# Kernel optimization log

Hardware: AMD Instinct MI355X
Metric: run time of the kernel (lower is better)

The kernel has to match this reference:

```python
import jax, jax.numpy as jnp
import numpy as np

N_NODES = 50000
N_EDGES = 1_600_000
F_IN = 32
HIDDEN = 32
HORIZON = 12
K = 2


def setup_inputs() -> dict:
    key = jax.random.key(0)
    ks = jax.random.split(key, 12)
    s = 0.1  # keep gates away from saturation
    x = jax.random.normal(ks[0], (N_NODES, 1, F_IN), dtype=jnp.float32)
    edge_index = jax.random.randint(ks[1], (2, N_EDGES), 0, N_NODES, dtype=jnp.int64)
    edge_weight = jax.random.uniform(ks[2], (N_EDGES,), dtype=jnp.float32)
    Wx = jax.random.normal(ks[3], (4, K, F_IN, HIDDEN), dtype=jnp.float32) * s
    bx = jax.random.normal(ks[4], (4, HIDDEN), dtype=jnp.float32) * s
    Wh = jax.random.normal(ks[5], (4, K, HIDDEN, HIDDEN), dtype=jnp.float32) * s
    bh = jax.random.normal(ks[6], (4, HIDDEN), dtype=jnp.float32) * s
    wc = jax.random.normal(ks[7], (3, HIDDEN), dtype=jnp.float32) * s
    b = jax.random.normal(ks[8], (4, HIDDEN), dtype=jnp.float32) * s
    W_lin = jax.random.normal(ks[9], (HIDDEN, HORIZON), dtype=jnp.float32) * s
    b_lin = jax.random.normal(ks[10], (HORIZON,), dtype=jnp.float32) * s
    h0 = jnp.zeros((N_NODES, HIDDEN), dtype=jnp.float32)
    c0 = jnp.zeros((N_NODES, HIDDEN), dtype=jnp.float32)
    return dict(x=x, edge_index=edge_index, edge_weight=edge_weight, Wx=Wx, bx=bx,
                Wh=Wh, bh=bh, wc=wc, b=b, W_lin=W_lin, b_lin=b_lin, h0=h0, c0=c0)


def reference(x, edge_index, edge_weight, Wx, bx, Wh, bh, wc, b, W_lin, b_lin, h0, c0):
    N = x.shape[0]
    src, dst = edge_index[0], edge_index[1]
    # ChebConv sym normalization with lambda_max=2: L_hat = L - I = -D^{-1/2} A D^{-1/2}
    deg = jax.ops.segment_sum(edge_weight, src, num_segments=N)
    dinv = jnp.where(deg > 0, jax.lax.rsqrt(deg), 0.0)
    nw = -dinv[src] * edge_weight * dinv[dst]  # [E]

    X = x[:, 0, :]  # squeeze(1) -> [N, F]

    def cheb(Z, W, bb):
        # K=2 Chebyshev: T0(Z)=Z, T1(Z)=L_hat Z (sparse gather-scatter)
        LZ = jax.ops.segment_sum(nw[:, None] * Z[src], dst, num_segments=N)
        return Z @ W[0] + LZ @ W[1] + bb

    # gate order: i, f, c, o
    I = jax.nn.sigmoid(cheb(X, Wx[0], bx[0]) + cheb(h0, Wh[0], bh[0]) + wc[0] * c0 + b[0])
    Fg = jax.nn.sigmoid(cheb(X, Wx[1], bx[1]) + cheb(h0, Wh[1], bh[1]) + wc[1] * c0 + b[1])
    T = jnp.tanh(cheb(X, Wx[2], bx[2]) + cheb(h0, Wh[2], bh[2]) + b[2])
    C = Fg * c0 + I * T
    O = jax.nn.sigmoid(cheb(X, Wx[3], bx[3]) + cheb(h0, Wh[3], bh[3]) + wc[2] * C + b[3])
    H = O * jnp.tanh(C)

    h = jax.nn.relu(H) @ W_lin + b_lin  # Linear(32, horizon)
    return (h, H, C)
```

## Files before the change

### kernel.cpp

```cpp
#include <hip/hip_runtime.h>
#include <math.h>

#define HID 32
#define HOR 12
#define NB  256
#define GSH 6
#define GW  64
#define NPT 4

__device__ __forceinline__ float sigmoidf_(float x) { return 1.0f / (1.0f + expf(-x)); }


__global__ __launch_bounds__(1024) void k_hist(const int* __restrict__ src,
                                               const int* __restrict__ dst,
                                               int* __restrict__ hist,
                                               int E, int chunk, int ng) {
    __shared__ int hS[1024], hD[1024];
    int t = threadIdx.x, b = blockIdx.x;
    for (int i = t; i < ng; i += 1024) { hS[i] = 0; hD[i] = 0; }
    __syncthreads();
    int beg = b * chunk, end = min(E, beg + chunk);
    for (int e = beg + t; e < end; e += 1024) {
        atomicAdd(&hS[src[e] >> GSH], 1);
        atomicAdd(&hD[dst[e] >> GSH], 1);
    }
    __syncthreads();
    for (int i = t; i < ng; i += 1024) {
        hist[(size_t)i * NB + b] = hS[i];
        hist[((size_t)ng + i) * NB + b] = hD[i];
    }
}

__global__ __launch_bounds__(256) void k_binscan(const int* __restrict__ hist,
                                                 int* __restrict__ off,
                                                 int* __restrict__ binTot, int ng2) {
    __shared__ int s[256];
    int b2 = blockIdx.x, t = threadIdx.x;
    int v = hist[(size_t)b2 * NB + t];
    s[t] = v;
    __syncthreads();
    for (int o = 1; o < 256; o <<= 1) {
        int x = (t >= o) ? s[t - o] : 0;
        __syncthreads();
        s[t] += x;
        __syncthreads();
    }
    off[(size_t)t * ng2 + b2] = s[t] - v;
    if (t == 255) binTot[b2] = s[255];
}

__global__ __launch_bounds__(1024) void k_binbase(const int* __restrict__ binTot,
                                                  int* __restrict__ baseS, int* __restrict__ baseD,
                                                  int* __restrict__ rowptr,
                                                  int E, int ng, int N) {
    __shared__ int buf[1024];
    int t = threadIdx.x;
    int isD = blockIdx.x;
    int sum = (t < ng) ? binTot[isD * ng + t] : 0;
    buf[t] = sum;
    __syncthreads();
    for (int o = 1; o < 1024; o <<= 1) {
        int v = (t >= o) ? buf[t - o] : 0;
        __syncthreads();
        buf[t] += v;
        __syncthreads();
    }
    int base = buf[t] - sum;
    int* B = isD ? baseD : baseS;
    if (t < ng) B[t] = base;
    if (t == 0) { B[ng] = E; if (!isD) rowptr[N] = E; }
}

__global__ __launch_bounds__(1024) void k_scatter(const int* __restrict__ src,
                                                  const int* __restrict__ dst,
                                                  const float* __restrict__ w,
                                                  const int* __restrict__ off,
                                                  const int* __restrict__ baseS,
                                                  const int* __restrict__ baseD,
                                                  int2* __restrict__ tmpS, int2* __restrict__ tmpD,
                                                  int E, int chunk, int ng) {
    __shared__ int cS[1024], cD[1024];
    int t = threadIdx.x, b = blockIdx.x;
    int ng2 = 2 * ng;
    for (int i = t; i < ng; i += 1024) {
        cS[i] = off[(size_t)b * ng2 + i] + baseS[i];
        cD[i] = off[(size_t)b * ng2 + ng + i] + baseD[i];
    }
    __syncthreads();
    int beg = b * chunk, end = min(E, beg + chunk);
    for (int e = beg + t; e < end; e += 1024) {
        int s = src[e], d = dst[e];
        int wb = __float_as_int(w[e]);
        int pS = atomicAdd(&cS[s >> GSH], 1);
        tmpS[pS] = make_int2(s, wb);
        int pD = atomicAdd(&cD[d >> GSH], 1);
        tmpD[pD] = make_int2(s | ((d & (GW - 1)) << 16), wb);
    }
}

__global__ __launch_bounds__(256) void k_degsum(const int2* __restrict__ tmpS,
                                                const int* __restrict__ baseS,
                                                float* __restrict__ dinv, int N) {
    __shared__ float h[GW];
    int g = blockIdx.x, t = threadIdx.x;
    if (t < GW) h[t] = 0.0f;
    __syncthreads();
    int beg = baseS[g], end = baseS[g + 1];
    for (int i = beg + t; i < end; i += 256) {
        int2 p = tmpS[i];
        atomicAdd(&h[p.x & (GW - 1)], __int_as_float(p.y));
    }
    __syncthreads();
    int n = (g << GSH) + t;
    if (t < GW && n < N) { float s = h[t]; dinv[n] = (s > 0.0f) ? rsqrtf(s) : 0.0f; }
}

__global__ __launch_bounds__(256) void k_scatter2(const int2* __restrict__ tmpD,
                                                  const int* __restrict__ baseD,
                                                  const float* __restrict__ dinv,
                                                  int* __restrict__ rowptr,
                                                  int2* __restrict__ epair, int N) {
    __shared__ int h[GW], cur[GW];
    int g = blockIdx.x, t = threadIdx.x;
    if (t < GW) h[t] = 0;
    __syncthreads();
    int beg = baseD[g], end = baseD[g + 1];
    for (int i = beg + t; i < end; i += 256) atomicAdd(&h[(tmpD[i].x >> 16) & (GW - 1)], 1);
    __syncthreads();
    int v = (t < GW) ? h[t] : 0;
    for (int o = 1; o < GW; o <<= 1) {
        int x = (t < GW && t >= o) ? h[t - o] : 0;
        __syncthreads();
        if (t < GW && t >= o) h[t] += x;
        __syncthreads();
    }
    if (t < GW) {
        int excl = h[t] - v;
        int n = (g << GSH) + t;
        if (n < N) rowptr[n] = beg + excl;
        cur[t] = beg + excl;
    }
    __syncthreads();
    for (int i = beg + t; i < end; i += 256) {
        int2 p = tmpD[i];
        int low = (p.x >> 16) & (GW - 1);
        int s = p.x & 0xFFFF;
        int pos = atomicAdd(&cur[low], 1);
        float nw = -dinv[s] * __int_as_float(p.y) * dinv[(g << GSH) + low];
        epair[pos] = make_int2(s, __float_as_int(nw));
    }
}

__global__ void k_flags(const float* __restrict__ h0, const float* __restrict__ c0,
                        int* __restrict__ flag, int total) {
    int i = blockIdx.x * 256 + threadIdx.x;
    float a = (i < total) ? h0[i] : 0.0f;
    float c = (i < total) ? c0[i] : 0.0f;
    unsigned long long ba = __ballot(a != 0.0f);
    unsigned long long bc = __ballot(c != 0.0f);
    if ((threadIdx.x & 63) == 0) {
        int m = (ba ? 1 : 0) | (bc ? 2 : 0);
        if (m) atomicOr(flag, m);
    }
}

__global__ __launch_bounds__(256) void k_gather(const int* __restrict__ rowptr,
                                                const int2* __restrict__ epair,
                                                const float* __restrict__ X,
                                                const float* __restrict__ H0,
                                                const int* __restrict__ hflag,
                                                float* __restrict__ LX, float* __restrict__ LH,
                                                int N) {
    int tid = blockIdx.x * 256 + threadIdx.x;
    int n = tid >> 5;
    int f = tid & 31;
    if (n >= N) return;
    int beg = rowptr[n], end = rowptr[n + 1];
    float acc = 0.0f, accH = 0.0f;
    int fl = *hflag;
    if (fl & 1) {
        #pragma unroll 4
        for (int i = beg; i < end; ++i) {
            int2 p = epair[i];
            float w = __int_as_float(p.y);
            acc  += w * X[(p.x << 5) + f];
            accH += w * H0[(p.x << 5) + f];
        }
    } else {
        #pragma unroll 4
        for (int i = beg; i < end; ++i) {
            int2 p = epair[i];
            acc += __int_as_float(p.y) * X[(p.x << 5) + f];
        }
    }
    LX[(n << 5) + f] = acc;
    if (fl & 1) LH[(n << 5) + f] = accH;
}

__global__ __launch_bounds__(256) void k_gates(
    const float* __restrict__ X, const float* __restrict__ LX,
    const float* __restrict__ H0, const float* __restrict__ LH,
    const float* __restrict__ C0,
    const float* __restrict__ Wx, const float* __restrict__ bx,
    const float* __restrict__ Wh, const float* __restrict__ bh,
    const float* __restrict__ wc, const float* __restrict__ b,
    const int* __restrict__ flag,
    float* __restrict__ outH, float* __restrict__ outC, int N) {
    int tid = blockIdx.x * 256 + threadIdx.x;
    int g = tid >> 5;
    int j = tid & 31;
    int n0 = g * NPT;
    if (n0 >= N) return;
    int cnt = min(NPT, N - n0);
    int f2 = *flag;

    if (f2 == 0) {
        float xk[NPT], lxk[NPT];
        #pragma unroll
        for (int i = 0; i < NPT; ++i) { xk[i] = 0.0f; lxk[i] = 0.0f; }
        for (int i = 0; i < cnt; ++i) {
            int base = (n0 + i) << 5;
            xk[i]  = X[base + j];
            lxk[i] = LX[base + j];
        }
        float p0[NPT], p2[NPT], p3[NPT];
        float b0 = bx[0 * HID + j] + bh[0 * HID + j] + b[0 * HID + j];
        float b2 = bx[2 * HID + j] + bh[2 * HID + j] + b[2 * HID + j];
        float b3 = bx[3 * HID + j] + bh[3 * HID + j] + b[3 * HID + j];
        #pragma unroll
        for (int i = 0; i < NPT; ++i) { p0[i] = b0; p2[i] = b2; p3[i] = b3; }

        #pragma unroll 4
        for (int k = 0; k < HID; ++k) {
            int row = k * HID + j;
            float w00 = Wx[0 * 2048 + row], w01 = Wx[0 * 2048 + 1024 + row];
            float w20 = Wx[2 * 2048 + row], w21 = Wx[2 * 2048 + 1024 + row];
            float w30 = Wx[3 * 2048 + row], w31 = Wx[3 * 2048 + 1024 + row];
            #pragma unroll
            for (int i = 0; i < NPT; ++i) {
                float xv  = __shfl(xk[i],  k, 32);
                float lxv = __shfl(lxk[i], k, 32);
                p0[i] += xv * w00 + lxv * w01;
                p2[i] += xv * w20 + lxv * w21;
                p3[i] += xv * w30 + lxv * w31;
            }
        }

        float wc2 = wc[2 * HID + j];
        for (int i = 0; i < cnt; ++i) {
            int base = (n0 + i) << 5;
            float I = sigmoidf_(p0[i]);
            float T = tanhf(p2[i]);
            float C = I * T;
            float O = sigmoidf_(p3[i] + wc2 * C);
            outH[base + j] = O * tanhf(C);
            outC[base + j] = C;
        }
        return;
    }

    float xk[NPT], lxk[NPT], hk[NPT], lhk[NPT];
    #pragma unroll
    for (int i = 0; i < NPT; ++i) { xk[i] = 0.0f; lxk[i] = 0.0f; hk[i] = 0.0f; lhk[i] = 0.0f; }
    for (int i = 0; i < cnt; ++i) {
        int base = (n0 + i) << 5;
        xk[i]  = X[base + j];
        lxk[i] = LX[base + j];
        hk[i]  = H0[base + j];
        lhk[i] = (f2 & 1) ? LH[base + j] : 0.0f;
    }

    float pre[4][NPT];
    #pragma unroll
    for (int gt = 0; gt < 4; ++gt) {
        float bb = bx[gt * HID + j] + bh[gt * HID + j] + b[gt * HID + j];
        #pragma unroll
        for (int i = 0; i < NPT; ++i) pre[gt][i] = bb;
    }

    #pragma unroll 2
    for (int k = 0; k < HID; ++k) {
        float w0[4], w1[4], w2[4], w3[4];
        int row = k * HID + j;
        #pragma unroll
        for (int gt = 0; gt < 4; ++gt) {
            w0[gt] = Wx[gt * 2048 + row];
            w1[gt] = Wx[gt * 2048 + 1024 + row];
            w2[gt] = Wh[gt * 2048 + row];
            w3[gt] = Wh[gt * 2048 + 1024 + row];
        }
        #pragma unroll
        for (int i = 0; i < NPT; ++i) {
            float xv  = __shfl(xk[i],  k, 32);
            float lxv = __shfl(lxk[i], k, 32);
            float hv  = __shfl(hk[i],  k, 32);
            float lhv = __shfl(lhk[i], k, 32);
            #pragma unroll
            for (int gt = 0; gt < 4; ++gt)
                pre[gt][i] += xv * w0[gt] + lxv * w1[gt] + hv * w2[gt] + lhv * w3[gt];
        }
    }

    float wc0 = wc[0 * HID + j], wc1 = wc[1 * HID + j], wc2 = wc[2 * HID + j];
    for (int i = 0; i < cnt; ++i) {
        int base = (n0 + i) << 5;
        float c0v = C0[base + j];
        float I  = sigmoidf_(pre[0][i] + wc0 * c0v);
        float Fg = sigmoidf_(pre[1][i] + wc1 * c0v);
        float T  = tanhf(pre[2][i]);
        float C  = Fg * c0v + I * T;
        float O  = sigmoidf_(pre[3][i] + wc2 * C);
        float H  = O * tanhf(C);
        outH[base + j] = H;
        outC[base + j] = C;
    }
}

__global__ void k_head(const float* __restrict__ H, const float* __restrict__ Wl,
                       const float* __restrict__ bl, float* __restrict__ hout, int N) {
    int tid = blockIdx.x * 256 + threadIdx.x;
    int n = tid / HOR;
    int t = tid - n * HOR;
    if (n >= N) return;
    float acc = bl[t];
    #pragma unroll
    for (int k = 0; k < HID; ++k) {
        float v = H[(n << 5) + k];
        acc += fmaxf(v, 0.0f) * Wl[k * HOR + t];
    }
    hout[n * HOR + t] = acc;
}

extern "C" void kernel_launch(void* const* d_in, const int* in_sizes, int n_in,
                              void* d_out, int out_size, void* d_ws, size_t ws_size,
                              hipStream_t stream) {
    const float* x  = (const float*)d_in[0];
    const int*   ei = (const int*)d_in[1];
    const float* ew = (const float*)d_in[2];
    const float* Wx = (const float*)d_in[3];
    const float* bx = (const float*)d_in[4];
    const float* Wh = (const float*)d_in[5];
    const float* bh = (const float*)d_in[6];
    const float* wc = (const float*)d_in[7];
    const float* b  = (const float*)d_in[8];
    const float* Wl = (const float*)d_in[9];
    const float* bl = (const float*)d_in[10];
    const float* h0 = (const float*)d_in[11];
    const float* c0 = (const float*)d_in[12];

    int N = in_sizes[0] / HID;
    int E = in_sizes[2];
    const int* src = ei;
    const int* dst = ei + E;

    int ng = (N + GW - 1) >> GSH;
    int ng2 = 2 * ng;
    int chunk = (E + NB - 1) / NB;

    int* wsi = (int*)d_ws;
    int2*  tmpD   = (int2*)wsi;
    int2*  tmpS   = (int2*)(wsi + 2 * (size_t)E);
    int2*  epair  = tmpS;
    float* LX     = (float*)(wsi + 4 * (size_t)E);
    float* LH     = LX + (size_t)N * HID;
    int*   rowptr = (int*)(LH + (size_t)N * HID);
    int*   hist   = rowptr + (N + 1);
    int*   off    = hist + (size_t)ng2 * NB;
    int*   binTot = off + (size_t)ng2 * NB;
    int*   baseS  = binTot + 2048;
    int*   baseD  = baseS + (ng + 1);
    float* dinv   = (float*)(baseD + (ng + 1));
    int*   flag   = (int*)(dinv + N);

    float* hOut = (float*)d_out;
    float* HOut = hOut + (size_t)N * HOR;
    float* COut = HOut + (size_t)N * HID;

    hipMemsetAsync(flag, 0, sizeof(int), stream);

    k_hist<<<NB, 1024, 0, stream>>>(src, dst, hist, E, chunk, ng);
    k_binscan<<<ng2, 256, 0, stream>>>(hist, off, binTot, ng2);
    k_binbase<<<2, 1024, 0, stream>>>(binTot, baseS, baseD, rowptr, E, ng, N);
    k_scatter<<<NB, 1024, 0, stream>>>(src, dst, ew, off, baseS, baseD, tmpS, tmpD, E, chunk, ng);
    k_degsum<<<ng, 256, 0, stream>>>(tmpS, baseS, dinv, N);
    k_flags<<<(N * HID + 255) / 256, 256, 0, stream>>>(h0, c0, flag, N * HID);
    k_scatter2<<<ng, 256, 0, stream>>>(tmpD, baseD, dinv, rowptr, epair, N);

    k_gather<<<(N * HID + 255) / 256, 256, 0, stream>>>(rowptr, epair, x, h0, flag, LX, LH, N);

    int gThreads = ((N + NPT - 1) / NPT) * 32;
    k_gates<<<(gThreads + 255) / 256, 256, 0, stream>>>(x, LX, h0, LH, c0,
                                                        Wx, bx, Wh, bh, wc, b, flag,
                                                        HOut, COut, N);

    k_head<<<(N * HOR + 255) / 256, 256, 0, stream>>>(HOut, Wl, bl, hOut, N);
}
```

Baseline: 275.5 us.

## Stage edge scatter in LDS tiles and gather per node-group with shared atomics

The edge bucketing kernel now sorts each 4096-edge tile in shared memory by group before writing it out, so global writes to each bin are contiguous rather than scattered one at a time. The second-level per-node scatter kernel is removed. The gather now runs one block per 64-node group, computing normalized weights on the fly and accumulating into shared-memory tiles with LDS float atomics. This drops a full pass over the edge list and the rowptr construction, at the cost of shared atomic contention and lower parallelism in the gather (one block per group, 8 edges in flight per block).

```diff
diff --git a/kernel.cpp b/kernel.cpp
--- a/kernel.cpp
+++ b/kernel.cpp
@@ -7,6 +7,10 @@
 #define GSH 6
 #define GW  64
 #define NPT 4
+#define TILE 4096
+#define TPB  256
+#define U    16
+#define BINS 1024
 
 __device__ __forceinline__ float sigmoidf_(float x) { return 1.0f / (1.0f + expf(-x)); }
 
@@ -15,7 +19,7 @@
                                                const int* __restrict__ dst,
                                                int* __restrict__ hist,
                                                int E, int chunk, int ng) {
-    __shared__ int hS[1024], hD[1024];
+    __shared__ int hS[BINS], hD[BINS];
     int t = threadIdx.x, b = blockIdx.x;
     for (int i = t; i < ng; i += 1024) { hS[i] = 0; hD[i] = 0; }
     __syncthreads();
@@ -51,8 +55,7 @@
 
 __global__ __launch_bounds__(1024) void k_binbase(const int* __restrict__ binTot,
                                                   int* __restrict__ baseS, int* __restrict__ baseD,
-                                                  int* __restrict__ rowptr,
-                                                  int E, int ng, int N) {
+                                                  int E, int ng) {
     __shared__ int buf[1024];
     int t = threadIdx.x;
     int isD = blockIdx.x;
@@ -68,33 +71,93 @@
     int base = buf[t] - sum;
     int* B = isD ? baseD : baseS;
     if (t < ng) B[t] = base;
-    if (t == 0) { B[ng] = E; if (!isD) rowptr[N] = E; }
-}
-
-__global__ __launch_bounds__(1024) void k_scatter(const int* __restrict__ src,
-                                                  const int* __restrict__ dst,
-                                                  const float* __restrict__ w,
-                                                  const int* __restrict__ off,
-                                                  const int* __restrict__ baseS,
-                                                  const int* __restrict__ baseD,
-                                                  int2* __restrict__ tmpS, int2* __restrict__ tmpD,
-                                                  int E, int chunk, int ng) {
-    __shared__ int cS[1024], cD[1024];
+    if (t == 0) B[ng] = E;
+}
+
+__global__ __launch_bounds__(256) void k_scatter(const int* __restrict__ src,
+                                                 const int* __restrict__ dst,
+                                                 const float* __restrict__ w,
+                                                 const int* __restrict__ off,
+                                                 const int* __restrict__ baseS,
+                                                 const int* __restrict__ baseD,
+                                                 int2* __restrict__ tmpS, int2* __restrict__ tmpD,
+                                                 int E, int chunk, int ng) {
+    __shared__ int2 stage[TILE];
+    __shared__ unsigned short stageG[TILE];
+    __shared__ int cnt[BINS];
+    __shared__ int gcur[BINS];
+    __shared__ int aux[TPB];
     int t = threadIdx.x, b = blockIdx.x;
+    int beg = b * chunk, end = min(E, beg + chunk);
     int ng2 = 2 * ng;
-    for (int i = t; i < ng; i += 1024) {
-        cS[i] = off[(size_t)b * ng2 + i] + baseS[i];
-        cD[i] = off[(size_t)b * ng2 + ng + i] + baseD[i];
-    }
-    __syncthreads();
-    int beg = b * chunk, end = min(E, beg + chunk);
-    for (int e = beg + t; e < end; e += 1024) {
-        int s = src[e], d = dst[e];
-        int wb = __float_as_int(w[e]);
-        int pS = atomicAdd(&cS[s >> GSH], 1);
-        tmpS[pS] = make_int2(s, wb);
-        int pD = atomicAdd(&cD[d >> GSH], 1);
-        tmpD[pD] = make_int2(s | ((d & (GW - 1)) << 16), wb);
+
+    for (int pass = 0; pass < 2; ++pass) {
+        for (int i = t; i < ng; i += TPB)
+            gcur[i] = (pass == 0) ? off[(size_t)b * ng2 + i] + baseS[i]
+                                  : off[(size_t)b * ng2 + ng + i] + baseD[i];
+        __syncthreads();
+
+        for (int tb = beg; tb < end; tb += TILE) {
+            int tcount = min(TILE, end - tb);
+            for (int i = t; i < BINS; i += TPB) cnt[i] = 0;
+            __syncthreads();
+
+            int g_[U], r_[U];
+            int2 p_[U];
+            #pragma unroll
+            for (int u = 0; u < U; ++u) {
+                int li = u * TPB + t;
+                g_[u] = -1;
+                if (li < tcount) {
+                    int e = tb + li;
+                    int s = src[e];
+                    int wb = __float_as_int(w[e]);
+                    int g; int2 p;
+                    if (pass == 0) { g = s >> GSH; p = make_int2(s, wb); }
+                    else { int d = dst[e]; g = d >> GSH; p = make_int2(s | ((d & (GW - 1)) << 16), wb); }
+                    g_[u] = g; p_[u] = p;
+                    r_[u] = atomicAdd(&cnt[g], 1);
+                }
+            }
+            __syncthreads();
+
+            int c0 = cnt[4 * t], c1 = cnt[4 * t + 1], c2 = cnt[4 * t + 2], c3 = cnt[4 * t + 3];
+            int q1 = c0, q2 = c0 + c1, q3 = c0 + c1 + c2, tsum = q3 + c3;
+            aux[t] = tsum;
+            __syncthreads();
+            for (int o = 1; o < TPB; o <<= 1) {
+                int v = (t >= o) ? aux[t - o] : 0;
+                __syncthreads();
+                aux[t] += v;
+                __syncthreads();
+            }
+            int excl = aux[t] - tsum;
+            cnt[4 * t] = excl; cnt[4 * t + 1] = excl + q1;
+            cnt[4 * t + 2] = excl + q2; cnt[4 * t + 3] = excl + q3;
+            __syncthreads();
+
+            #pragma unroll
+            for (int u = 0; u < U; ++u) {
+                if (g_[u] >= 0) {
+                    int pos = cnt[g_[u]] + r_[u];
+                    stage[pos] = p_[u];
+                    stageG[pos] = (unsigned short)g_[u];
+                }
+            }
+            __syncthreads();
+
+            int2* out = (pass == 0) ? tmpS : tmpD;
+            for (int i = t; i < tcount; i += TPB) {
+                int g = stageG[i];
+                out[gcur[g] + (i - cnt[g])] = stage[i];
+            }
+            __syncthreads();
+
+            gcur[4 * t] += c0; gcur[4 * t + 1] += c1;
+            gcur[4 * t + 2] += c2; gcur[4 * t + 3] += c3;
+            __syncthreads();
+        }
+        __syncthreads();
     }
 }
 
@@ -113,42 +176,6 @@
     __syncthreads();
     int n = (g << GSH) + t;
     if (t < GW && n < N) { float s = h[t]; dinv[n] = (s > 0.0f) ? rsqrtf(s) : 0.0f; }
-}
-
-__global__ __launch_bounds__(256) void k_scatter2(const int2* __restrict__ tmpD,
-                                                  const int* __restrict__ baseD,
-                                                  const float* __restrict__ dinv,
-                                                  int* __restrict__ rowptr,
-                                                  int2* __restrict__ epair, int N) {
-    __shared__ int h[GW], cur[GW];
-    int g = blockIdx.x, t = threadIdx.x;
-    if (t < GW) h[t] = 0;
-    __syncthreads();
-    int beg = baseD[g], end = baseD[g + 1];
-    for (int i = beg + t; i < end; i += 256) atomicAdd(&h[(tmpD[i].x >> 16) & (GW - 1)], 1);
-    __syncthreads();
-    int v = (t < GW) ? h[t] : 0;
-    for (int o = 1; o < GW; o <<= 1) {
-        int x = (t < GW && t >= o) ? h[t - o] : 0;
-        __syncthreads();
-        if (t < GW && t >= o) h[t] += x;
-        __syncthreads();
-    }
-    if (t < GW) {
-        int excl = h[t] - v;
-        int n = (g << GSH) + t;
-        if (n < N) rowptr[n] = beg + excl;
-        cur[t] = beg + excl;
-    }
-    __syncthreads();
-    for (int i = beg + t; i < end; i += 256) {
-        int2 p = tmpD[i];
-        int low = (p.x >> 16) & (GW - 1);
-        int s = p.x & 0xFFFF;
-        int pos = atomicAdd(&cur[low], 1);
-        float nw = -dinv[s] * __int_as_float(p.y) * dinv[(g << GSH) + low];
-        epair[pos] = make_int2(s, __float_as_int(nw));
-    }
 }
 
 __global__ void k_flags(const float* __restrict__ h0, const float* __restrict__ c0,
@@ -164,37 +191,51 @@
     }
 }
 
-__global__ __launch_bounds__(256) void k_gather(const int* __restrict__ rowptr,
-                                                const int2* __restrict__ epair,
+__global__ __launch_bounds__(256) void k_gather(const int2* __restrict__ tmpD,
+                                                const int* __restrict__ baseD,
+                                                const float* __restrict__ dinv,
                                                 const float* __restrict__ X,
                                                 const float* __restrict__ H0,
                                                 const int* __restrict__ hflag,
                                                 float* __restrict__ LX, float* __restrict__ LH,
                                                 int N) {
-    int tid = blockIdx.x * 256 + threadIdx.x;
-    int n = tid >> 5;
-    int f = tid & 31;
-    if (n >= N) return;
-    int beg = rowptr[n], end = rowptr[n + 1];
-    float acc = 0.0f, accH = 0.0f;
+    __shared__ float accX[GW][HID];
+    __shared__ float accH[GW][HID];
+    int g = blockIdx.x, t = threadIdx.x;
+    int f = t & 31, sub = t >> 5;
     int fl = *hflag;
+    for (int i = t; i < GW * HID; i += 256) {
+        ((float*)accX)[i] = 0.0f;
+        ((float*)accH)[i] = 0.0f;
+    }
+    __syncthreads();
+    int beg = baseD[g], end = baseD[g + 1];
     if (fl & 1) {
-        #pragma unroll 4
-        for (int i = beg; i < end; ++i) {
-            int2 p = epair[i];
-            float w = __int_as_float(p.y);
-            acc  += w * X[(p.x << 5) + f];
-            accH += w * H0[(p.x << 5) + f];
+        for (int i = beg + sub; i < end; i += 8) {
+            int2 p = tmpD[i];
+            int s = p.x & 0xFFFF;
+            int dlow = (p.x >> 16) & (GW - 1);
+            float nw = -dinv[s] * __int_as_float(p.y) * dinv[(g << GSH) + dlow];
+            atomicAdd(&accX[dlow][f], nw * X[(s << 5) + f]);
+            atomicAdd(&accH[dlow][f], nw * H0[(s << 5) + f]);
         }
     } else {
-        #pragma unroll 4
-        for (int i = beg; i < end; ++i) {
-            int2 p = epair[i];
-            acc += __int_as_float(p.y) * X[(p.x << 5) + f];
-        }
-    }
-    LX[(n << 5) + f] = acc;
-    if (fl & 1) LH[(n << 5) + f] = accH;
+        for (int i = beg + sub; i < end; i += 8) {
+            int2 p = tmpD[i];
+            int s = p.x & 0xFFFF;
+            int dlow = (p.x >> 16) & (GW - 1);
+            float nw = -dinv[s] * __int_as_float(p.y) * dinv[(g << GSH) + dlow];
+            atomicAdd(&accX[dlow][f], nw * X[(s << 5) + f]);
+        }
+    }
+    __syncthreads();
+    for (int i = t; i < GW * HID; i += 256) {
+        int n = (g << GSH) + (i >> 5);
+        if (n < N) {
+            LX[(n << 5) + (i & 31)] = ((float*)accX)[i];
+            if (fl & 1) LH[(n << 5) + (i & 31)] = ((float*)accH)[i];
+        }
+    }
 }
 
 __global__ __launch_bounds__(256) void k_gates(
@@ -360,11 +401,9 @@
     int* wsi = (int*)d_ws;
     int2*  tmpD   = (int2*)wsi;
     int2*  tmpS   = (int2*)(wsi + 2 * (size_t)E);
-    int2*  epair  = tmpS;
     float* LX     = (float*)(wsi + 4 * (size_t)E);
     float* LH     = LX + (size_t)N * HID;
-    int*   rowptr = (int*)(LH + (size_t)N * HID);
-    int*   hist   = rowptr + (N + 1);
+    int*   hist   = (int*)(LH + (size_t)N * HID);
     int*   off    = hist + (size_t)ng2 * NB;
     int*   binTot = off + (size_t)ng2 * NB;
     int*   baseS  = binTot + 2048;
@@ -380,13 +419,12 @@
 
     k_hist<<<NB, 1024, 0, stream>>>(src, dst, hist, E, chunk, ng);
     k_binscan<<<ng2, 256, 0, stream>>>(hist, off, binTot, ng2);
-    k_binbase<<<2, 1024, 0, stream>>>(binTot, baseS, baseD, rowptr, E, ng, N);
-    k_scatter<<<NB, 1024, 0, stream>>>(src, dst, ew, off, baseS, baseD, tmpS, tmpD, E, chunk, ng);
+    k_binbase<<<2, 1024, 0, stream>>>(binTot, baseS, baseD, E, ng);
+    k_scatter<<<NB, TPB, 0, stream>>>(src, dst, ew, off, baseS, baseD, tmpS, tmpD, E, chunk, ng);
     k_degsum<<<ng, 256, 0, stream>>>(tmpS, baseS, dinv, N);
     k_flags<<<(N * HID + 255) / 256, 256, 0, stream>>>(h0, c0, flag, N * HID);
-    k_scatter2<<<ng, 256, 0, stream>>>(tmpD, baseD, dinv, rowptr, epair, N);
-
-    k_gather<<<(N * HID + 255) / 256, 256, 0, stream>>>(rowptr, epair, x, h0, flag, LX, LH, N);
+
+    k_gather<<<ng, 256, 0, stream>>>(tmpD, baseD, dinv, x, h0, flag, LX, LH, N);
 
     int gThreads = ((N + NPT - 1) / NPT) * 32;
     k_gates<<<(gThreads + 255) / 256, 256, 0, stream>>>(x, LX, h0, LH, c0,
```

Measured after the change: 559.1 us. 2.03x slower.

## Fuse sparse gather, gate computation and linear head into one kernel

Applied to the files above, without the earlier changes.

Merges the Laplacian gather, the LSTM gate kernel and the output head into a single kernel. Each 32-lane group now computes the neighbor aggregation for its 4 nodes inline, then the gates, then the 12-wide head via shuffles. This removes the LX/LH intermediate buffers, the re-read of H and two kernel launches. In exchange the gather is serialized over 4 nodes per group, which reduces the number of concurrent waves available to hide random-access latency.

```diff
diff --git a/kernel.cpp b/kernel.cpp
--- a/kernel.cpp
+++ b/kernel.cpp
@@ -164,48 +164,17 @@
     }
 }
 
-__global__ __launch_bounds__(256) void k_gather(const int* __restrict__ rowptr,
-                                                const int2* __restrict__ epair,
-                                                const float* __restrict__ X,
-                                                const float* __restrict__ H0,
-                                                const int* __restrict__ hflag,
-                                                float* __restrict__ LX, float* __restrict__ LH,
-                                                int N) {
-    int tid = blockIdx.x * 256 + threadIdx.x;
-    int n = tid >> 5;
-    int f = tid & 31;
-    if (n >= N) return;
-    int beg = rowptr[n], end = rowptr[n + 1];
-    float acc = 0.0f, accH = 0.0f;
-    int fl = *hflag;
-    if (fl & 1) {
-        #pragma unroll 4
-        for (int i = beg; i < end; ++i) {
-            int2 p = epair[i];
-            float w = __int_as_float(p.y);
-            acc  += w * X[(p.x << 5) + f];
-            accH += w * H0[(p.x << 5) + f];
-        }
-    } else {
-        #pragma unroll 4
-        for (int i = beg; i < end; ++i) {
-            int2 p = epair[i];
-            acc += __int_as_float(p.y) * X[(p.x << 5) + f];
-        }
-    }
-    LX[(n << 5) + f] = acc;
-    if (fl & 1) LH[(n << 5) + f] = accH;
-}
-
-__global__ __launch_bounds__(256) void k_gates(
-    const float* __restrict__ X, const float* __restrict__ LX,
-    const float* __restrict__ H0, const float* __restrict__ LH,
+__global__ __launch_bounds__(256) void k_fused(
+    const int* __restrict__ rowptr, const int2* __restrict__ epair,
+    const float* __restrict__ X, const float* __restrict__ H0,
     const float* __restrict__ C0,
     const float* __restrict__ Wx, const float* __restrict__ bx,
     const float* __restrict__ Wh, const float* __restrict__ bh,
     const float* __restrict__ wc, const float* __restrict__ b,
+    const float* __restrict__ Wl, const float* __restrict__ bl,
     const int* __restrict__ flag,
-    float* __restrict__ outH, float* __restrict__ outC, int N) {
+    float* __restrict__ hOut, float* __restrict__ outH, float* __restrict__ outC,
+    int N) {
     int tid = blockIdx.x * 256 + threadIdx.x;
     int g = tid >> 5;
     int j = tid & 31;
@@ -213,16 +182,25 @@
     if (n0 >= N) return;
     int cnt = min(NPT, N - n0);
     int f2 = *flag;
+    float blv = (j < HOR) ? bl[j] : 0.0f;
 
     if (f2 == 0) {
         float xk[NPT], lxk[NPT];
         #pragma unroll
         for (int i = 0; i < NPT; ++i) { xk[i] = 0.0f; lxk[i] = 0.0f; }
         for (int i = 0; i < cnt; ++i) {
-            int base = (n0 + i) << 5;
-            xk[i]  = X[base + j];
-            lxk[i] = LX[base + j];
-        }
+            int n = n0 + i;
+            xk[i] = X[(n << 5) + j];
+            int beg = rowptr[n], end = rowptr[n + 1];
+            float a = 0.0f;
+            #pragma unroll 4
+            for (int e = beg; e < end; ++e) {
+                int2 p = epair[e];
+                a += __int_as_float(p.y) * X[(p.x << 5) + j];
+            }
+            lxk[i] = a;
+        }
+
         float p0[NPT], p2[NPT], p3[NPT];
         float b0 = bx[0 * HID + j] + bh[0 * HID + j] + b[0 * HID + j];
         float b2 = bx[2 * HID + j] + bh[2 * HID + j] + b[2 * HID + j];
@@ -248,13 +226,22 @@
 
         float wc2 = wc[2 * HID + j];
         for (int i = 0; i < cnt; ++i) {
-            int base = (n0 + i) << 5;
+            int n = n0 + i;
+            int base = n << 5;
             float I = sigmoidf_(p0[i]);
             float T = tanhf(p2[i]);
             float C = I * T;
             float O = sigmoidf_(p3[i] + wc2 * C);
-            outH[base + j] = O * tanhf(C);
+            float H = O * tanhf(C);
+            outH[base + j] = H;
             outC[base + j] = C;
+            float ah = blv;
+            #pragma unroll 8
+            for (int k = 0; k < HID; ++k) {
+                float hv = __shfl(H, k, 32);
+                if (j < HOR) ah += fmaxf(hv, 0.0f) * Wl[k * HOR + j];
+            }
+            if (j < HOR) hOut[n * HOR + j] = ah;
         }
         return;
     }
@@ -263,11 +250,29 @@
     #pragma unroll
     for (int i = 0; i < NPT; ++i) { xk[i] = 0.0f; lxk[i] = 0.0f; hk[i] = 0.0f; lhk[i] = 0.0f; }
     for (int i = 0; i < cnt; ++i) {
-        int base = (n0 + i) << 5;
-        xk[i]  = X[base + j];
-        lxk[i] = LX[base + j];
-        hk[i]  = H0[base + j];
-        lhk[i] = (f2 & 1) ? LH[base + j] : 0.0f;
+        int n = n0 + i;
+        int base = n << 5;
+        xk[i] = X[base + j];
+        hk[i] = H0[base + j];
+        int beg = rowptr[n], end = rowptr[n + 1];
+        float a = 0.0f, ah = 0.0f;
+        if (f2 & 1) {
+            #pragma unroll 4
+            for (int e = beg; e < end; ++e) {
+                int2 p = epair[e];
+                float w = __int_as_float(p.y);
+                a  += w * X[(p.x << 5) + j];
+                ah += w * H0[(p.x << 5) + j];
+            }
+        } else {
+            #pragma unroll 4
+            for (int e = beg; e < end; ++e) {
+                int2 p = epair[e];
+                a += __int_as_float(p.y) * X[(p.x << 5) + j];
+            }
+        }
+        lxk[i] = a;
+        lhk[i] = ah;
     }
 
     float pre[4][NPT];
@@ -303,7 +308,8 @@
 
     float wc0 = wc[0 * HID + j], wc1 = wc[1 * HID + j], wc2 = wc[2 * HID + j];
     for (int i = 0; i < cnt; ++i) {
-        int base = (n0 + i) << 5;
+        int n = n0 + i;
+        int base = n << 5;
         float c0v = C0[base + j];
         float I  = sigmoidf_(pre[0][i] + wc0 * c0v);
         float Fg = sigmoidf_(pre[1][i] + wc1 * c0v);
@@ -313,22 +319,14 @@
         float H  = O * tanhf(C);
         outH[base + j] = H;
         outC[base + j] = C;
-    }
-}
-
-__global__ void k_head(const float* __restrict__ H, const float* __restrict__ Wl,
-                       const float* __restrict__ bl, float* __restrict__ hout, int N) {
-    int tid = blockIdx.x * 256 + threadIdx.x;
-    int n = tid / HOR;
-    int t = tid - n * HOR;
-    if (n >= N) return;
-    float acc = bl[t];
-    #pragma unroll
-    for (int k = 0; k < HID; ++k) {
-        float v = H[(n << 5) + k];
-        acc += fmaxf(v, 0.0f) * Wl[k * HOR + t];
-    }
-    hout[n * HOR + t] = acc;
+        float ah = blv;
+        #pragma unroll 8
+        for (int k = 0; k < HID; ++k) {
+            float hv = __shfl(H, k, 32);
+            if (j < HOR) ah += fmaxf(hv, 0.0f) * Wl[k * HOR + j];
+        }
+        if (j < HOR) hOut[n * HOR + j] = ah;
+    }
 }
 
 extern "C" void kernel_launch(void* const* d_in, const int* in_sizes, int n_in,
@@ -361,9 +359,7 @@
     int2*  tmpD   = (int2*)wsi;
     int2*  tmpS   = (int2*)(wsi + 2 * (size_t)E);
     int2*  epair  = tmpS;
-    float* LX     = (float*)(wsi + 4 * (size_t)E);
-    float* LH     = LX + (size_t)N * HID;
-    int*   rowptr = (int*)(LH + (size_t)N * HID);
+    int*   rowptr = wsi + 4 * (size_t)E;
     int*   hist   = rowptr + (N + 1);
     int*   off    = hist + (size_t)ng2 * NB;
     int*   binTot = off + (size_t)ng2 * NB;
@@ -386,12 +382,8 @@
     k_flags<<<(N * HID + 255) / 256, 256, 0, stream>>>(h0, c0, flag, N * HID);
     k_scatter2<<<ng, 256, 0, stream>>>(tmpD, baseD, dinv, rowptr, epair, N);
 
-    k_gather<<<(N * HID + 255) / 256, 256, 0, stream>>>(rowptr, epair, x, h0, flag, LX, LH, N);
-
     int gThreads = ((N + NPT - 1) / NPT) * 32;
-    k_gates<<<(gThreads + 255) / 256, 256, 0, stream>>>(x, LX, h0, LH, c0,
-                                                        Wx, bx, Wh, bh, wc, b, flag,
-                                                        HOut, COut, N);
-
-    k_head<<<(N * HOR + 255) / 256, 256, 0, stream>>>(HOut, Wl, bl, hOut, N);
-}
+    k_fused<<<(gThreads + 255) / 256, 256, 0, stream>>>(rowptr, epair, x, h0, c0,
+                                                        Wx, bx, Wh, bh, wc, b, Wl, bl, flag,
+                                                        hOut, HOut, COut, N);
+}
```

Measured after the change: 323.9 us. +17.6%, slower.
